# Kernel tuning notes

Hardware: AMD Instinct MI355X
Metric: run time of the kernel (lower is better)

## Reference

```python
import jax, jax.numpy as jnp
import numpy as np

B, T, N, M, D = 4, 2, 2048, 2048, 3

def _pairwise_sq(a, b):
    # a: [B,N,D], b: [B,M,D] -> squared euclidean distances [B,N,M]
    a2 = jnp.sum(a * a, axis=-1)
    b2 = jnp.sum(b * b, axis=-1)
    ab = jnp.einsum('bnd,bmd->bnm', a, b)
    return jnp.maximum(a2[:, :, None] + b2[:, None, :] - 2.0 * ab, 0.0)


def setup_inputs() -> dict:
    key = jax.random.key(0)
    k1, k2, k3, k4 = jax.random.split(key, 4)
    x = jax.random.uniform(k1, (B, T, N, D), dtype=jnp.float32)
    # m_hat is the frozen motion model's output; small motions keep chamfer mask active
    m_hat = jax.random.uniform(k2, (B, 1, N, D), dtype=jnp.float32) * 0.02
    y_hat0 = jax.random.uniform(k3, (B, 1, M, D), dtype=jnp.float32)
    y_hat1 = jax.random.uniform(k4, (B, 1, M, D), dtype=jnp.float32)
    return {'x': x, 'm_hat': m_hat, 'y_hat0': y_hat0, 'y_hat1': y_hat1}


def reference(x, m_hat, y_hat0, y_hat1):
    sg = jax.lax.stop_gradient
    x_t0 = x[:, 0, :, :3]              # [B,N,3]
    x_t1 = x[:, 1, :, :3]              # [B,N,3]
    x_t1_hat = x_t0 + m_hat[:, 0]      # [B,N,3]

    # chamfer(x_t1_hat, x_t1): squared NN distances both ways
    d = _pairwise_sq(x_t1_hat, x_t1)   # [B,N,N]
    dist1 = jnp.min(d, axis=-1)
    dist2 = jnp.min(d, axis=-2)
    loss_chamfer = dist1.mean(axis=-1) + dist2.mean(axis=-1)          # [B]
    mask_chamfer = sg((loss_chamfer < 0.1).astype(x.dtype))[:, None, None, None]

    y0 = y_hat0[:, 0]                  # [B,M,3]
    dists = jnp.sqrt(_pairwise_sq(y0, x_t0))                          # [B,M,N]
    x_cat = jnp.concatenate([x_t0, x_t1], axis=1)                     # [B,2N,3]
    dists2 = jnp.sqrt(_pairwise_sq(y0, x_cat))                        # [B,M,2N]

    min_dists = jnp.min(dists, axis=-1)        # [B,M]
    min_indices = jnp.argmin(dists, axis=-1)   # [B,M]
    min_dists2 = jnp.min(dists2, axis=-1)      # [B,M]

    mask_dist = sg((min_dists < 0.05).astype(x.dtype))[:, None, :, None]      # [B,1,M,1]
    mask_dist_neg = sg((min_dists2 > 0.2).astype(x.dtype))[:, None, :, None]  # [B,1,M,1]

    nearest_m = jnp.take_along_axis(m_hat[:, 0], min_indices[:, :, None], axis=1)  # [B,M,3]

    # chamfer(x_t0, y_hat0): only dist1 used, masked mean over entries < 0.1
    c1 = jnp.min(_pairwise_sq(x_t0, y0), axis=-1)                     # [B,N]
    sel = c1 < 0.1
    loss_dist = jnp.sum(jnp.where(sel, c1, 0.0)) / jnp.maximum(jnp.sum(sel.astype(c1.dtype)), 1.0)

    pred = (y_hat1 - y_hat0) * mask_chamfer * mask_dist               # [B,1,M,3]
    tgt = nearest_m[:, None, :, :] * mask_chamfer * mask_dist
    loss_dynamic = jnp.mean((pred - tgt) ** 2)

    my_hat_static = (y_hat1 - y_hat0) * mask_dist_neg
    loss_static = jnp.mean(my_hat_static ** 2)

    return (loss_dynamic, loss_static, loss_dist)
```

## Files before the change

kernel.cpp:

```cpp
#include <hip/hip_runtime.h>
#include <math.h>

#define BATCH 4
#define NPTS  2048
#define NT    256
#define ROWS_PT 4
#define CPB     64
#define COLCHUNKS (NPTS / CPB)
#define ROWHALVES 2
#define ROWS_TOT  (BATCH * NPTS)

#define OFF_PD1   0
#define OFF_PD2   (COLCHUNKS * ROWS_TOT)
#define OFF_PC1   (2 * COLCHUNKS * ROWS_TOT)
#define OFF_PRM3  (3 * COLCHUNKS * ROWS_TOT)
#define OFF_PRM2  (4 * COLCHUNKS * ROWS_TOT)
#define OFF_BLK   (6 * COLCHUNKS * ROWS_TOT)

#define INF_BITS 0x7f800000u

typedef unsigned long long ull;

__device__ __forceinline__ float sqnorm3(float x, float y, float z) {
    return __fadd_rn(__fadd_rn(__fmul_rn(x, x), __fmul_rn(y, y)), __fmul_rn(z, z));
}

#define SRC_T0  0
#define SRC_T1  1
#define SRC_T1H 2
#define SRC_Y0  3

__device__ __forceinline__ float4 make_point(int src, int b, int i,
    const float* __restrict__ x, const float* __restrict__ m_hat,
    const float* __restrict__ y_hat0)
{
    float px, py, pz;
    if (src == SRC_Y0) {
        const float* p = y_hat0 + ((size_t)b * NPTS + i) * 3;
        px = p[0]; py = p[1]; pz = p[2];
    } else if (src == SRC_T1) {
        const float* p = x + ((size_t)(b * 2 + 1) * NPTS + i) * 3;
        px = p[0]; py = p[1]; pz = p[2];
    } else {
        const float* p = x + ((size_t)(b * 2 + 0) * NPTS + i) * 3;
        px = p[0]; py = p[1]; pz = p[2];
        if (src == SRC_T1H) {
            const float* mh = m_hat + ((size_t)b * NPTS + i) * 3;
            px += mh[0]; py += mh[1]; pz += mh[2];
        }
    }
    return make_float4(px, py, pz, sqnorm3(px, py, pz));
}

__device__ __forceinline__ ull shfl_xor_u64(ull v, int m) {
    int lo = __shfl_xor((int)(v & 0xFFFFFFFFull), m);
    int hi = __shfl_xor((int)(v >> 32), m);
    return ((ull)(unsigned)hi << 32) | (unsigned)lo;
}

__global__ __launch_bounds__(NT) void pairwise_kernel(
    const float* __restrict__ x, const float* __restrict__ m_hat,
    const float* __restrict__ y_hat0, float* __restrict__ ws)
{
    __shared__ float4 tile[CPB];

    int tid = threadIdx.x;
    int rowHalf  = blockIdx.x >> 5;
    int colChunk = blockIdx.x & 31;
    int b    = blockIdx.y;
    int prob = blockIdx.z;

    int rsrc, csrc, outOff;
    switch (prob) {
        case 0:  rsrc = SRC_T1H; csrc = SRC_T1;  outOff = OFF_PD1;  break;
        case 1:  rsrc = SRC_T1;  csrc = SRC_T1H; outOff = OFF_PD2;  break;
        case 2:  rsrc = SRC_Y0;  csrc = SRC_T0;  outOff = -1;       break;
        case 3:  rsrc = SRC_Y0;  csrc = SRC_T1;  outOff = OFF_PRM3; break;
        default: rsrc = SRC_T0;  csrc = SRC_Y0;  outOff = OFF_PC1;  break;
    }

    int colBase = colChunk * CPB;
    if (tid < CPB) tile[tid] = make_point(csrc, b, colBase + tid, x, m_hat, y_hat0);

    int r0 = rowHalf * (NT * ROWS_PT) + tid;
    float4 a[ROWS_PT];
    #pragma unroll
    for (int k = 0; k < ROWS_PT; ++k)
        a[k] = make_point(rsrc, b, r0 + k * NT, x, m_hat, y_hat0);

    __syncthreads();

    if (prob == 2) {
        float best[ROWS_PT];
        int bestIdx[ROWS_PT];
        #pragma unroll
        for (int k = 0; k < ROWS_PT; ++k) { best[k] = __uint_as_float(INF_BITS); bestIdx[k] = 0; }
        #pragma unroll 4
        for (int c = 0; c < CPB; ++c) {
            float4 q = tile[c];
            #pragma unroll
            for (int k = 0; k < ROWS_PT; ++k) {
                float dot = a[k].x * q.x + a[k].y * q.y + a[k].z * q.z;
                float d = __fsub_rn(__fadd_rn(a[k].w, q.w), __fmul_rn(2.0f, dot));
                d = fmaxf(d, 0.0f);
                if (d < best[k]) { best[k] = d; bestIdx[k] = c; }
            }
        }
        ull* prm2 = (ull*)(ws + OFF_PRM2);
        #pragma unroll
        for (int k = 0; k < ROWS_PT; ++k) {
            ull key = ((ull)__float_as_uint(best[k]) << 32) |
                      (unsigned)(colBase + bestIdx[k]);
            prm2[(size_t)colChunk * ROWS_TOT + b * NPTS + r0 + k * NT] = key;
        }
    } else {
        float best[ROWS_PT];
        #pragma unroll
        for (int k = 0; k < ROWS_PT; ++k) best[k] = __uint_as_float(INF_BITS);
        #pragma unroll 4
        for (int c = 0; c < CPB; ++c) {
            float4 q = tile[c];
            #pragma unroll
            for (int k = 0; k < ROWS_PT; ++k) {
                float dot = a[k].x * q.x + a[k].y * q.y + a[k].z * q.z;
                float d = __fsub_rn(__fadd_rn(a[k].w, q.w), __fmul_rn(2.0f, dot));
                d = fmaxf(d, 0.0f);
                best[k] = fminf(best[k], d);
            }
        }
        #pragma unroll
        for (int k = 0; k < ROWS_PT; ++k)
            ws[outOff + (size_t)colChunk * ROWS_TOT + b * NPTS + r0 + k * NT] = best[k];
    }
}

__global__ __launch_bounds__(NT) void rowreduce_kernel(
    const float* __restrict__ m_hat, const float* __restrict__ y_hat0,
    const float* __restrict__ y_hat1, float* __restrict__ ws)
{
    int tid  = threadIdx.x;
    int row  = blockIdx.x * 128 + (tid >> 1);
    int half = tid & 1;
    int b    = row >> 11;

    const ull* prm2 = (const ull*)(ws + OFF_PRM2);

    float d1m = __uint_as_float(INF_BITS), d2m = d1m, c1m = d1m, r3m = d1m;
    ull k2 = ~0ull;
    #pragma unroll
    for (int c = 0; c < 16; ++c) {
        int idx = (half * 16 + c) * ROWS_TOT + row;
        d1m = fminf(d1m, ws[OFF_PD1 + idx]);
        d2m = fminf(d2m, ws[OFF_PD2 + idx]);
        c1m = fminf(c1m, ws[OFF_PC1 + idx]);
        r3m = fminf(r3m, ws[OFF_PRM3 + idx]);
        ull kk = prm2[idx];
        k2 = (kk < k2) ? kk : k2;
    }
    d1m = fminf(d1m, __shfl_xor(d1m, 1));
    d2m = fminf(d2m, __shfl_xor(d2m, 1));
    c1m = fminf(c1m, __shfl_xor(c1m, 1));
    r3m = fminf(r3m, __shfl_xor(r3m, 1));
    { ull o = shfl_xor_u64(k2, 1); k2 = (o < k2) ? o : k2; }

    float d2sq = __uint_as_float((unsigned)(k2 >> 32));
    unsigned idxm = (unsigned)(k2 & 0xFFFFFFFFull);
    float md   = (sqrtf(d2sq) < 0.05f) ? 1.0f : 0.0f;
    float dcat = fminf(d2sq, r3m);
    float mneg = (sqrtf(dcat) > 0.2f) ? 1.0f : 0.0f;

    const float* p0 = y_hat0 + (size_t)row * 3;
    const float* p1 = y_hat1 + (size_t)row * 3;
    const float* nm = m_hat + ((size_t)b * NPTS + idxm) * 3;

    float dyn = 0.f, stat = 0.f;
    #pragma unroll
    for (int k = 0; k < 3; ++k) {
        float diff = p1[k] - p0[k];
        float e = md * (diff - nm[k]);
        dyn += e * e;
        float s = mneg * diff;
        stat += s * s;
    }
    float cs = (c1m < 0.1f) ? c1m : 0.f;
    float cn = (c1m < 0.1f) ? 1.f  : 0.f;
    float s1 = d1m, s2 = d2m;
    if (half) { s1 = s2 = cs = cn = dyn = stat = 0.f; }

    #pragma unroll
    for (int off = 32; off > 0; off >>= 1) {
        s1  += __shfl_down(s1,  off);
        s2  += __shfl_down(s2,  off);
        cs  += __shfl_down(cs,  off);
        cn  += __shfl_down(cn,  off);
        dyn += __shfl_down(dyn, off);
        stat+= __shfl_down(stat,off);
    }
    __shared__ float sm[4][6];
    int wv = tid >> 6, ln = tid & 63;
    if (ln == 0) {
        sm[wv][0] = s1; sm[wv][1] = s2; sm[wv][2] = cs;
        sm[wv][3] = cn; sm[wv][4] = dyn; sm[wv][5] = stat;
    }
    __syncthreads();
    if (tid == 0) {
        #pragma unroll
        for (int j = 0; j < 6; ++j)
            ws[OFF_BLK + blockIdx.x * 8 + j] = sm[0][j] + sm[1][j] + sm[2][j] + sm[3][j];
    }
}

__global__ void final_kernel(const float* __restrict__ ws, float* __restrict__ out)
{
    int lane = threadIdx.x;
    float v[6];
    #pragma unroll
    for (int j = 0; j < 6; ++j) v[j] = ws[OFF_BLK + lane * 8 + j];
    #pragma unroll
    for (int off = 8; off > 0; off >>= 1) {
        #pragma unroll
        for (int j = 0; j < 6; ++j) {
            float t = __shfl_down(v[j], off);
            if (((lane & 15) + off) < 16) v[j] += t;
        }
    }
    __shared__ float bs[4][6];
    if ((lane & 15) == 0) {
        #pragma unroll
        for (int j = 0; j < 6; ++j) bs[lane >> 4][j] = v[j];
    }
    __syncthreads();
    if (lane == 0) {
        float dyn = 0.f, stat = 0.f, cs = 0.f, cn = 0.f;
        for (int b = 0; b < 4; ++b) {
            float lc = bs[b][0] / (float)NPTS + bs[b][1] / (float)NPTS;
            float maskc = (lc < 0.1f) ? 1.0f : 0.0f;
            dyn  += maskc * bs[b][4];
            stat += bs[b][5];
            cs   += bs[b][2];
            cn   += bs[b][3];
        }
        const float denom = (float)(BATCH * NPTS * 3);
        out[0] = dyn / denom;
        out[1] = stat / denom;
        out[2] = cs / fmaxf(cn, 1.0f);
    }
}

extern "C" void kernel_launch(void* const* d_in, const int* in_sizes, int n_in,
                              void* d_out, int out_size, void* d_ws, size_t ws_size,
                              hipStream_t stream)
{
    const float* x      = (const float*)d_in[0];
    const float* m_hat  = (const float*)d_in[1];
    const float* y_hat0 = (const float*)d_in[2];
    const float* y_hat1 = (const float*)d_in[3];
    float* ws  = (float*)d_ws;
    float* out = (float*)d_out;

    pairwise_kernel<<<dim3(ROWHALVES * COLCHUNKS, BATCH, 5), dim3(NT), 0, stream>>>(
        x, m_hat, y_hat0, ws);
    rowreduce_kernel<<<dim3(ROWS_TOT / 128), dim3(NT), 0, stream>>>(
        m_hat, y_hat0, y_hat1, ws);
    final_kernel<<<dim3(1), dim3(64), 0, stream>>>(ws, out);
}
```

Before: 86.43 us.

## Fold final reduction into last rowreduce block and prescale column points by -2

Drops the separate final kernel launch. The last rowreduce block to finish, detected through an atomic counter that the pairwise kernel resets, now does the final cross-block reduction. Column points are also pre-multiplied by -2, so the inner distance loop avoids one multiply and a subtract per pair. The prescaling may change floating-point rounding slightly versus the reference expression. The last-block pattern depends on threadfence ordering and uses a wait-count builtin rather than a barrier before reading shared memory.

New measurement: 87.56 us. No clear change (+1.3%).

```diff
diff --git a/kernel.cpp b/kernel.cpp
--- a/kernel.cpp
+++ b/kernel.cpp
@@ -9,6 +9,7 @@
 #define COLCHUNKS (NPTS / CPB)
 #define ROWHALVES 2
 #define ROWS_TOT  (BATCH * NPTS)
+#define RB_BLOCKS (ROWS_TOT / 128)
 
 #define OFF_PD1   0
 #define OFF_PD2   (COLCHUNKS * ROWS_TOT)
@@ -16,6 +17,7 @@
 #define OFF_PRM3  (3 * COLCHUNKS * ROWS_TOT)
 #define OFF_PRM2  (4 * COLCHUNKS * ROWS_TOT)
 #define OFF_BLK   (6 * COLCHUNKS * ROWS_TOT)
+#define OFF_CNT   (OFF_BLK + RB_BLOCKS * 32)
 
 #define INF_BITS 0x7f800000u
 
@@ -30,7 +32,7 @@
 #define SRC_T1H 2
 #define SRC_Y0  3
 
-__device__ __forceinline__ float4 make_point(int src, int b, int i,
+__device__ __forceinline__ float4 make_point(int src, bool col, int b, int i,
     const float* __restrict__ x, const float* __restrict__ m_hat,
     const float* __restrict__ y_hat0)
 {
@@ -49,7 +51,9 @@
             px += mh[0]; py += mh[1]; pz += mh[2];
         }
     }
-    return make_float4(px, py, pz, sqnorm3(px, py, pz));
+    float w = sqnorm3(px, py, pz);
+    if (col) { px *= -2.0f; py *= -2.0f; pz *= -2.0f; }
+    return make_float4(px, py, pz, w);
 }
 
 __device__ __forceinline__ ull shfl_xor_u64(ull v, int m) {
@@ -69,6 +73,9 @@
     int colChunk = blockIdx.x & 31;
     int b    = blockIdx.y;
     int prob = blockIdx.z;
+
+    if (blockIdx.x == 0 && b == 0 && prob == 0 && tid == 0)
+        ((unsigned*)ws)[OFF_CNT] = 0u;
 
     int rsrc, csrc, outOff;
     switch (prob) {
@@ -80,13 +87,13 @@
     }
 
     int colBase = colChunk * CPB;
-    if (tid < CPB) tile[tid] = make_point(csrc, b, colBase + tid, x, m_hat, y_hat0);
+    if (tid < CPB) tile[tid] = make_point(csrc, true, b, colBase + tid, x, m_hat, y_hat0);
 
     int r0 = rowHalf * (NT * ROWS_PT) + tid;
     float4 a[ROWS_PT];
     #pragma unroll
     for (int k = 0; k < ROWS_PT; ++k)
-        a[k] = make_point(rsrc, b, r0 + k * NT, x, m_hat, y_hat0);
+        a[k] = make_point(rsrc, false, b, r0 + k * NT, x, m_hat, y_hat0);
 
     __syncthreads();
 
@@ -100,9 +107,9 @@
             float4 q = tile[c];
             #pragma unroll
             for (int k = 0; k < ROWS_PT; ++k) {
-                float dot = a[k].x * q.x + a[k].y * q.y + a[k].z * q.z;
-                float d = __fsub_rn(__fadd_rn(a[k].w, q.w), __fmul_rn(2.0f, dot));
-                d = fmaxf(d, 0.0f);
+                float s = a[k].x * q.x + a[k].y * q.y + a[k].z * q.z;
+                float u = __fadd_rn(a[k].w, q.w);
+                float d = fmaxf(__fadd_rn(u, s), 0.0f);
                 if (d < best[k]) { best[k] = d; bestIdx[k] = c; }
             }
         }
@@ -122,9 +129,9 @@
             float4 q = tile[c];
             #pragma unroll
             for (int k = 0; k < ROWS_PT; ++k) {
-                float dot = a[k].x * q.x + a[k].y * q.y + a[k].z * q.z;
-                float d = __fsub_rn(__fadd_rn(a[k].w, q.w), __fmul_rn(2.0f, dot));
-                d = fmaxf(d, 0.0f);
+                float s = a[k].x * q.x + a[k].y * q.y + a[k].z * q.z;
+                float u = __fadd_rn(a[k].w, q.w);
+                float d = fmaxf(__fadd_rn(u, s), 0.0f);
                 best[k] = fminf(best[k], d);
             }
         }
@@ -136,7 +143,7 @@
 
 __global__ __launch_bounds__(NT) void rowreduce_kernel(
     const float* __restrict__ m_hat, const float* __restrict__ y_hat0,
-    const float* __restrict__ y_hat1, float* __restrict__ ws)
+    const float* __restrict__ y_hat1, float* __restrict__ ws, float* __restrict__ out)
 {
     int tid  = threadIdx.x;
     int row  = blockIdx.x * 128 + (tid >> 1);
@@ -203,47 +210,54 @@
         sm[wv][3] = cn; sm[wv][4] = dyn; sm[wv][5] = stat;
     }
     __syncthreads();
+
+    __shared__ int sLast;
     if (tid == 0) {
         #pragma unroll
         for (int j = 0; j < 6; ++j)
-            ws[OFF_BLK + blockIdx.x * 8 + j] = sm[0][j] + sm[1][j] + sm[2][j] + sm[3][j];
-    }
-}
-
-__global__ void final_kernel(const float* __restrict__ ws, float* __restrict__ out)
-{
-    int lane = threadIdx.x;
-    float v[6];
-    #pragma unroll
-    for (int j = 0; j < 6; ++j) v[j] = ws[OFF_BLK + lane * 8 + j];
-    #pragma unroll
-    for (int off = 8; off > 0; off >>= 1) {
-        #pragma unroll
-        for (int j = 0; j < 6; ++j) {
-            float t = __shfl_down(v[j], off);
-            if (((lane & 15) + off) < 16) v[j] += t;
-        }
-    }
-    __shared__ float bs[4][6];
-    if ((lane & 15) == 0) {
-        #pragma unroll
-        for (int j = 0; j < 6; ++j) bs[lane >> 4][j] = v[j];
+            ws[OFF_BLK + blockIdx.x * 32 + j] = sm[0][j] + sm[1][j] + sm[2][j] + sm[3][j];
+        __threadfence();
+        unsigned old = atomicAdd((unsigned*)ws + OFF_CNT, 1u);
+        sLast = (old == RB_BLOCKS - 1) ? 1 : 0;
     }
     __syncthreads();
-    if (lane == 0) {
-        float dyn = 0.f, stat = 0.f, cs = 0.f, cn = 0.f;
-        for (int b = 0; b < 4; ++b) {
-            float lc = bs[b][0] / (float)NPTS + bs[b][1] / (float)NPTS;
-            float maskc = (lc < 0.1f) ? 1.0f : 0.0f;
-            dyn  += maskc * bs[b][4];
-            stat += bs[b][5];
-            cs   += bs[b][2];
-            cn   += bs[b][3];
-        }
-        const float denom = (float)(BATCH * NPTS * 3);
-        out[0] = dyn / denom;
-        out[1] = stat / denom;
-        out[2] = cs / fmaxf(cn, 1.0f);
+    if (!sLast) return;
+
+    __threadfence();
+    int lane = tid;
+    if (lane < 64) {
+        float v[6];
+        #pragma unroll
+        for (int j = 0; j < 6; ++j) v[j] = ws[OFF_BLK + lane * 32 + j];
+        #pragma unroll
+        for (int off = 8; off > 0; off >>= 1) {
+            #pragma unroll
+            for (int j = 0; j < 6; ++j) {
+                float t = __shfl_down(v[j], off);
+                if (((lane & 15) + off) < 16) v[j] += t;
+            }
+        }
+        __shared__ float bs[4][6];
+        if ((lane & 15) == 0) {
+            #pragma unroll
+            for (int j = 0; j < 6; ++j) bs[lane >> 4][j] = v[j];
+        }
+        __builtin_amdgcn_s_waitcnt(0);
+        if (lane == 0) {
+            float dyn = 0.f, stat = 0.f, cs = 0.f, cn = 0.f;
+            for (int bb = 0; bb < 4; ++bb) {
+                float lc = bs[bb][0] / (float)NPTS + bs[bb][1] / (float)NPTS;
+                float maskc = (lc < 0.1f) ? 1.0f : 0.0f;
+                dyn  += maskc * bs[bb][4];
+                stat += bs[bb][5];
+                cs   += bs[bb][2];
+                cn   += bs[bb][3];
+            }
+            const float denom = (float)(BATCH * NPTS * 3);
+            out[0] = dyn / denom;
+            out[1] = stat / denom;
+            out[2] = cs / fmaxf(cn, 1.0f);
+        }
     }
 }
 
@@ -260,7 +274,6 @@
 
     pairwise_kernel<<<dim3(ROWHALVES * COLCHUNKS, BATCH, 5), dim3(NT), 0, stream>>>(
         x, m_hat, y_hat0, ws);
-    rowreduce_kernel<<<dim3(ROWS_TOT / 128), dim3(NT), 0, stream>>>(
-        m_hat, y_hat0, y_hat1, ws);
-    final_kernel<<<dim3(1), dim3(64), 0, stream>>>(ws, out);
-}
+    rowreduce_kernel<<<dim3(RB_BLOCKS), dim3(NT), 0, stream>>>(
+        m_hat, y_hat0, y_hat1, ws, out);
+}
```
